# Kernel optimization log

Hardware: AMD Instinct MI355X
Metric: run time of the kernel (lower is better)

Reference implementation:

```python
import jax, jax.numpy as jnp
import numpy as np

B, S, D, H, DFF = 2, 2048, 1024, 16, 4096
DK = D // H
EPS = 1e-5


def layer_norm(x, gamma, beta, eps=EPS):
    mu = jnp.mean(x, axis=-1, keepdims=True)
    var = jnp.mean(jnp.square(x - mu), axis=-1, keepdims=True)
    return (x - mu) * jax.lax.rsqrt(var + eps) * gamma + beta


def setup_inputs() -> dict:
    key = jax.random.key(0)
    ks = jax.random.split(key, 12)
    s_d = 1.0 / np.sqrt(D)
    s_f = 1.0 / np.sqrt(DFF)
    return {
        "x": jax.random.normal(ks[0], (B, S, D), jnp.float32),
        # per-head QKV projections stacked: [H, D, DK]
        "Wq": jax.random.normal(ks[1], (H, D, DK), jnp.float32) * s_d,
        "bq": jnp.zeros((H, DK), jnp.float32),
        "Wk": jax.random.normal(ks[2], (H, D, DK), jnp.float32) * s_d,
        "bk": jnp.zeros((H, DK), jnp.float32),
        "Wv": jax.random.normal(ks[3], (H, D, DK), jnp.float32) * s_d,
        "bv": jnp.zeros((H, DK), jnp.float32),
        "Wo": jax.random.normal(ks[4], (D, D), jnp.float32) * s_d,
        "bo": jnp.zeros((D,), jnp.float32),
        "W1": jax.random.normal(ks[5], (D, DFF), jnp.float32) * s_d,
        "b1": jnp.zeros((DFF,), jnp.float32),
        "W2": jax.random.normal(ks[6], (DFF, D), jnp.float32) * s_f,
        "b2": jnp.zeros((D,), jnp.float32),
        "ln1_g": jnp.ones((D,), jnp.float32),
        "ln1_b": jnp.zeros((D,), jnp.float32),
        "ln2_g": jnp.ones((D,), jnp.float32),
        "ln2_b": jnp.zeros((D,), jnp.float32),
    }


def reference(x, Wq, bq, Wk, bk, Wv, bv, Wo, bo, W1, b1, W2, b2,
              ln1_g, ln1_b, ln2_g, ln2_b):
    # --- residual 1: pre-norm multi-head self-attention (mask unused, dropout=eval) ---
    h = layer_norm(x, ln1_g, ln1_b)                      # [B,S,D]
    q = jnp.einsum('bsd,hdk->bhsk', h, Wq) + bq[:, None, :]
    k = jnp.einsum('bsd,hdk->bhsk', h, Wk) + bk[:, None, :]
    v = jnp.einsum('bsd,hdk->bhsk', h, Wv) + bv[:, None, :]
    scores = jnp.einsum('bhsk,bhtk->bhst', q, k) / np.sqrt(DK)  # [B,H,S,S]
    w = jax.nn.softmax(scores, axis=-1)
    ctx = jnp.einsum('bhst,bhtk->bhsk', w, v)            # [B,H,S,DK]
    # concat heads along feature dim -> [B,S,D]
    ctx = jnp.transpose(ctx, (0, 2, 1, 3)).reshape(B, S, D)
    attn_out = ctx @ Wo + bo
    x = x + attn_out
    # --- residual 2: pre-norm feed-forward ---
    h2 = layer_norm(x, ln2_g, ln2_b)
    ff = jax.nn.relu(h2 @ W1 + b1) @ W2 + b2
    return x + ff
```

## Files before the change

kernel.cpp:

```cpp
#include <hip/hip_runtime.h>

#define B_   2
#define S_   2048
#define D_   1024
#define H_   16
#define DK_  64
#define DFF_ 4096
#define NT_  (B_*S_)
#define QS_  3072

using u16 = unsigned short;
typedef __attribute__((ext_vector_type(8))) short bf16x8;
typedef __attribute__((ext_vector_type(4))) float f32x4;
typedef __attribute__((ext_vector_type(4))) u16  u16x4;

__device__ __forceinline__ float bf2f(u16 h) {
  union { unsigned u; float f; } c; c.u = ((unsigned)h) << 16; return c.f;
}
__device__ __forceinline__ u16 f2bf(float f) {
  union { float f; unsigned u; } c; c.f = f;
  unsigned u = c.u;
  return (u16)((u + 0x7fffu + ((u >> 16) & 1u)) >> 16);
}
__device__ __forceinline__ u16 f2bf_up(float f) {
  union { float f; unsigned u; } c; c.f = f;
  return (u16)((c.u + 0x8000u) >> 16);
}

__device__ __forceinline__ void load_lds16(const void* g, void* l) {
  __builtin_amdgcn_global_load_lds(
      (const __attribute__((address_space(1))) unsigned int*)g,
      (__attribute__((address_space(3))) unsigned int*)l, 16, 0, 0);
}

__device__ __forceinline__ void store_out(u16* p, float v)   { *p = f2bf(v); }
__device__ __forceinline__ void store_out(float* p, float v) { *p = v; }

__global__ __launch_bounds__(256) void ln_kernel(
    const float* __restrict__ x, const float* __restrict__ g,
    const float* __restrict__ bt, u16* __restrict__ o)
{
  const int row = blockIdx.x, t = threadIdx.x;
  const float4 xv = *(const float4*)(x + (size_t)row * D_ + t * 4);
  float f[4] = {xv.x, xv.y, xv.z, xv.w};
  float sum = f[0] + f[1] + f[2] + f[3];
  float sq  = f[0]*f[0] + f[1]*f[1] + f[2]*f[2] + f[3]*f[3];
#pragma unroll
  for (int d = 32; d >= 1; d >>= 1) {
    sum += __shfl_down(sum, d);
    sq  += __shfl_down(sq, d);
  }
  __shared__ float red[8];
  const int lane = t & 63, wid = t >> 6;
  if (lane == 0) { red[wid] = sum; red[wid + 4] = sq; }
  __syncthreads();
  sum = red[0] + red[1] + red[2] + red[3];
  sq  = red[4] + red[5] + red[6] + red[7];
  const float mu   = sum * (1.0f / D_);
  const float var  = sq * (1.0f / D_) - mu * mu;
  const float rstd = rsqrtf(var + 1e-5f);
  const float4 gv = *(const float4*)(g  + t * 4);
  const float4 bv = *(const float4*)(bt + t * 4);
  u16x4 ov;
  ov[0] = f2bf((f[0] - mu) * rstd * gv.x + bv.x);
  ov[1] = f2bf((f[1] - mu) * rstd * gv.y + bv.y);
  ov[2] = f2bf((f[2] - mu) * rstd * gv.z + bv.z);
  ov[3] = f2bf((f[3] - mu) * rstd * gv.w + bv.w);
  *(u16x4*)(o + (size_t)row * D_ + t * 4) = ov;
}

__global__ __launch_bounds__(256) void transpose_h(
    const float* __restrict__ in, u16* __restrict__ out, int R, int C)
{
  __shared__ float tile[32][33];
  const int z = blockIdx.z;
  const float* ip = in  + (size_t)z * R * C;
  u16*         op = out + (size_t)z * R * C;
  const int c0 = blockIdx.x * 32, r0 = blockIdx.y * 32;
  const int tx = threadIdx.x & 31, ty = threadIdx.x >> 5;
#pragma unroll
  for (int i = 0; i < 32; i += 8)
    tile[ty + i][tx] = ip[(size_t)(r0 + ty + i) * C + c0 + tx];
  __syncthreads();
#pragma unroll
  for (int i = 0; i < 32; i += 8)
    op[(size_t)(c0 + ty + i) * R + r0 + tx] = f2bf(tile[tx][ty + i]);
}

__global__ __launch_bounds__(256) void transpose_qkv(
    const float* __restrict__ Wq, const float* __restrict__ Wk,
    const float* __restrict__ Wv, u16* __restrict__ out)
{
  __shared__ float tile[32][33];
  const int z = blockIdx.z;
  const int which = z >> 4, h = z & 15;
  const float* ip = (which == 0 ? Wq : which == 1 ? Wk : Wv) + (size_t)h * 1024 * 64;
  u16* op = out + ((size_t)which * 1024 + h * 64) * 1024;
  const float sc = (which == 0) ? 0.125f : 1.0f;
  const int c0 = blockIdx.x * 32, r0 = blockIdx.y * 32;
  const int tx = threadIdx.x & 31, ty = threadIdx.x >> 5;
#pragma unroll
  for (int i = 0; i < 32; i += 8)
    tile[ty + i][tx] = ip[(size_t)(r0 + ty + i) * 64 + c0 + tx];
  __syncthreads();
#pragma unroll
  for (int i = 0; i < 32; i += 8)
    op[(size_t)(c0 + ty + i) * 1024 + r0 + tx] = f2bf(tile[tx][ty + i] * sc);
}

__global__ __launch_bounds__(256) void transpose_v(
    const u16* __restrict__ qkv, u16* __restrict__ vt)
{
  __shared__ u16 tile[32][33];
  const int z = blockIdx.z;
  const int b = z >> 4, h = z & 15;
  const u16* ip = qkv + (size_t)(b * S_) * QS_ + 2048 + h * DK_;
  u16* op = vt + (size_t)z * DK_ * S_;
  const int t0 = blockIdx.x * 32, d0 = blockIdx.y * 32;
  const int tx = threadIdx.x & 31, ty = threadIdx.x >> 5;
#pragma unroll
  for (int i = 0; i < 32; i += 8)
    tile[ty + i][tx] = ip[(size_t)(t0 + ty + i) * QS_ + d0 + tx];
  __syncthreads();
#pragma unroll
  for (int i = 0; i < 32; i += 8)
    op[(size_t)(d0 + ty + i) * S_ + t0 + tx] = tile[tx][ty + i];
}

template <typename OT, int KK>
__global__ __launch_bounds__(512, 1) void gemm256(
    const u16* __restrict__ A, const u16* __restrict__ Bt,
    const float* __restrict__ bias, const float* __restrict__ biasB,
    const float* __restrict__ biasC, OT* __restrict__ C,
    int M, int N, int do_relu)
{
  constexpr int NK = KK / 32;
  __shared__ u16 lA[4][256 * 32];
  __shared__ u16 lB[4][256 * 32];
  const int tid = threadIdx.x, lane = tid & 63, wid = tid >> 6;
  const int wr = wid >> 2, wc = wid & 3;

  const int nbx = gridDim.x;
  int bid = blockIdx.y * nbx + blockIdx.x;
  const int cpx = (nbx * gridDim.y) >> 3;
  bid = (bid & 7) * cpx + (bid >> 3);
  const int row0 = (bid / nbx) * 256, col0 = (bid % nbx) * 256;

  const int c0 = tid,       sr0 = c0 >> 2, q0 = ((c0 & 3) ^ (((sr0 >> 3) & 1) << 1)) * 8;
  const int c1 = tid + 512, sr1 = c1 >> 2, q1 = ((c1 & 3) ^ (((sr1 >> 3) & 1) << 1)) * 8;
  const u16* As0 = A  + (size_t)(row0 + sr0) * KK + q0;
  const u16* As1 = A  + (size_t)(row0 + sr1) * KK + q1;
  const u16* Bs0 = Bt + (size_t)(col0 + sr0) * KK + q0;
  const u16* Bs1 = Bt + (size_t)(col0 + sr1) * KK + q1;

  f32x4 acc[8][4] = {};
  const int lrow = lane & 15, kcol = (lane >> 4) * 8;

#pragma unroll
  for (int t = 0; t < 3; ++t) {
    load_lds16(As0 + t * 32, &lA[t][c0 * 8]);
    load_lds16(Bs0 + t * 32, &lB[t][c0 * 8]);
    load_lds16(As1 + t * 32, &lA[t][c1 * 8]);
    load_lds16(Bs1 + t * 32, &lB[t][c1 * 8]);
  }
  asm volatile("s_waitcnt vmcnt(8)" ::: "memory");
  __builtin_amdgcn_sched_barrier(0);
  __builtin_amdgcn_s_barrier();

#pragma unroll 4
  for (int j = 0; j < NK; ++j) {
    const int b = j & 3;
    const u16* la = lA[b];
    const u16* lb = lB[b];
    bf16x8 af[4], bfr[4];

#pragma unroll
    for (int m = 0; m < 4; ++m) {
      const int row = wr * 128 + m * 16 + lrow;
      af[m] = *(const bf16x8*)&la[row * 32 + (kcol ^ (((row >> 3) & 1) << 4))];
    }
#pragma unroll
    for (int n = 0; n < 4; ++n) {
      const int row = wc * 64 + n * 16 + lrow;
      bfr[n] = *(const bf16x8*)&lb[row * 32 + (kcol ^ (((row >> 3) & 1) << 4))];
    }
    if (j + 3 < NK) {
      const int bb = (j + 3) & 3;
      load_lds16(As0 + (j + 3) * 32, &lA[bb][c0 * 8]);
      load_lds16(Bs0 + (j + 3) * 32, &lB[bb][c0 * 8]);
    }
    __builtin_amdgcn_s_setprio(1);
#pragma unroll
    for (int m = 0; m < 4; ++m)
#pragma unroll
      for (int n = 0; n < 4; ++n)
        acc[m][n] = __builtin_amdgcn_mfma_f32_16x16x32_bf16(af[m], bfr[n], acc[m][n], 0, 0, 0);
    __builtin_amdgcn_s_setprio(0);
    __builtin_amdgcn_sched_barrier(0);
    __builtin_amdgcn_s_barrier();

#pragma unroll
    for (int m = 0; m < 4; ++m) {
      const int row = wr * 128 + (m + 4) * 16 + lrow;
      af[m] = *(const bf16x8*)&la[row * 32 + (kcol ^ (((row >> 3) & 1) << 4))];
    }
    if (j + 3 < NK) {
      const int bb = (j + 3) & 3;
      load_lds16(As1 + (j + 3) * 32, &lA[bb][c1 * 8]);
      load_lds16(Bs1 + (j + 3) * 32, &lB[bb][c1 * 8]);
    }
    __builtin_amdgcn_s_setprio(1);
#pragma unroll
    for (int m = 0; m < 4; ++m)
#pragma unroll
      for (int n = 0; n < 4; ++n)
        acc[m + 4][n] = __builtin_amdgcn_mfma_f32_16x16x32_bf16(af[m], bfr[n], acc[m + 4][n], 0, 0, 0);
    __builtin_amdgcn_s_setprio(0);
    if (j + 3 < NK)      { asm volatile("s_waitcnt vmcnt(8)" ::: "memory"); }
    else if (j + 2 < NK) { asm volatile("s_waitcnt vmcnt(4)" ::: "memory"); }
    else if (j + 1 < NK) { asm volatile("s_waitcnt vmcnt(0)" ::: "memory"); }
    __builtin_amdgcn_sched_barrier(0);
    __builtin_amdgcn_s_barrier();
  }

#pragma unroll
  for (int m = 0; m < 8; ++m)
#pragma unroll
    for (int n = 0; n < 4; ++n) {
      const int rbase = row0 + wr*128 + m*16 + ((lane >> 4) << 2);
      const int c     = col0 + wc*64 + n*16 + (lane & 15);
      float bv = 0.f;
      if (biasC)      bv = c < 1024 ? bias[c] * 0.125f
                         : (c < 2048 ? biasB[c - 1024] : biasC[c - 2048]);
      else if (bias)  bv = bias[c];
#pragma unroll
      for (int r = 0; r < 4; ++r) {
        float vv = acc[m][n][r] + bv;
        if (do_relu) vv = vv > 0.f ? vv : 0.f;
        store_out(&C[(size_t)(rbase + r) * N + c], vv);
      }
    }
}

template <int KK>
__global__ __launch_bounds__(512, 1) void gemm256pk(
    const u16* __restrict__ A, const u16* __restrict__ Bt,
    u16* __restrict__ P, int M, int N, int Ktot)
{
  constexpr int NK = KK / 32;
  __shared__ u16 lA[4][256 * 32];
  __shared__ u16 lB[4][256 * 32];
  const int tid = threadIdx.x, lane = tid & 63, wid = tid >> 6;
  const int wr = wid >> 2, wc = wid & 3;

  const int nbx = gridDim.x;
  int bid = blockIdx.y * nbx + blockIdx.x;
  const int cpx = (nbx * gridDim.y) >> 3;
  bid = (bid & 7) * cpx + (bid >> 3);
  const int row0 = (bid / nbx) * 256, col0 = (bid % nbx) * 256;
  const int kb = blockIdx.z * KK;

  const int c0 = tid,       sr0 = c0 >> 2, q0 = ((c0 & 3) ^ (((sr0 >> 3) & 1) << 1)) * 8;
  const int c1 = tid + 512, sr1 = c1 >> 2, q1 = ((c1 & 3) ^ (((sr1 >> 3) & 1) << 1)) * 8;
  const u16* As0 = A  + (size_t)(row0 + sr0) * Ktot + kb + q0;
  const u16* As1 = A  + (size_t)(row0 + sr1) * Ktot + kb + q1;
  const u16* Bs0 = Bt + (size_t)(col0 + sr0) * Ktot + kb + q0;
  const u16* Bs1 = Bt + (size_t)(col0 + sr1) * Ktot + kb + q1;

  f32x4 acc[8][4] = {};
  const int lrow = lane & 15, kcol = (lane >> 4) * 8;

#pragma unroll
  for (int t = 0; t < 3; ++t) {
    load_lds16(As0 + t * 32, &lA[t][c0 * 8]);
    load_lds16(Bs0 + t * 32, &lB[t][c0 * 8]);
    load_lds16(As1 + t * 32, &lA[t][c1 * 8]);
    load_lds16(Bs1 + t * 32, &lB[t][c1 * 8]);
  }
  asm volatile("s_waitcnt vmcnt(8)" ::: "memory");
  __builtin_amdgcn_sched_barrier(0);
  __builtin_amdgcn_s_barrier();

#pragma unroll 4
  for (int j = 0; j < NK; ++j) {
    const int b = j & 3;
    const u16* la = lA[b];
    const u16* lb = lB[b];
    bf16x8 af[4], bfr[4];

#pragma unroll
    for (int m = 0; m < 4; ++m) {
      const int row = wr * 128 + m * 16 + lrow;
      af[m] = *(const bf16x8*)&la[row * 32 + (kcol ^ (((row >> 3) & 1) << 4))];
    }
#pragma unroll
    for (int n = 0; n < 4; ++n) {
      const int row = wc * 64 + n * 16 + lrow;
      bfr[n] = *(const bf16x8*)&lb[row * 32 + (kcol ^ (((row >> 3) & 1) << 4))];
    }
    if (j + 3 < NK) {
      const int bb = (j + 3) & 3;
      load_lds16(As0 + (j + 3) * 32, &lA[bb][c0 * 8]);
      load_lds16(Bs0 + (j + 3) * 32, &lB[bb][c0 * 8]);
    }
    __builtin_amdgcn_s_setprio(1);
#pragma unroll
    for (int m = 0; m < 4; ++m)
#pragma unroll
      for (int n = 0; n < 4; ++n)
        acc[m][n] = __builtin_amdgcn_mfma_f32_16x16x32_bf16(af[m], bfr[n], acc[m][n], 0, 0, 0);
    __builtin_amdgcn_s_setprio(0);
    __builtin_amdgcn_sched_barrier(0);
    __builtin_amdgcn_s_barrier();

#pragma unroll
    for (int m = 0; m < 4; ++m) {
      const int row = wr * 128 + (m + 4) * 16 + lrow;
      af[m] = *(const bf16x8*)&la[row * 32 + (kcol ^ (((row >> 3) & 1) << 4))];
    }
    if (j + 3 < NK) {
      const int bb = (j + 3) & 3;
      load_lds16(As1 + (j + 3) * 32, &lA[bb][c1 * 8]);
      load_lds16(Bs1 + (j + 3) * 32, &lB[bb][c1 * 8]);
    }
    __builtin_amdgcn_s_setprio(1);
#pragma unroll
    for (int m = 0; m < 4; ++m)
#pragma unroll
      for (int n = 0; n < 4; ++n)
        acc[m + 4][n] = __builtin_amdgcn_mfma_f32_16x16x32_bf16(af[m], bfr[n], acc[m + 4][n], 0, 0, 0);
    __builtin_amdgcn_s_setprio(0);
    if (j + 3 < NK)      { asm volatile("s_waitcnt vmcnt(8)" ::: "memory"); }
    else if (j + 2 < NK) { asm volatile("s_waitcnt vmcnt(4)" ::: "memory"); }
    else if (j + 1 < NK) { asm volatile("s_waitcnt vmcnt(0)" ::: "memory"); }
    __builtin_amdgcn_sched_barrier(0);
    __builtin_amdgcn_s_barrier();
  }

  u16* Pz = P + (size_t)blockIdx.z * M * N;
#pragma unroll
  for (int m = 0; m < 8; ++m)
#pragma unroll
    for (int n = 0; n < 4; ++n) {
      const int rbase = row0 + wr*128 + m*16 + ((lane >> 4) << 2);
      const int c     = col0 + wc*64 + n*16 + (lane & 15);
#pragma unroll
      for (int r = 0; r < 4; ++r)
        Pz[(size_t)(rbase + r) * N + c] = f2bf(acc[m][n][r]);
    }
}

template <typename OT>
__global__ __launch_bounds__(256) void gemm_bt64(
    const u16* __restrict__ A, const u16* __restrict__ Bt,
    const float* __restrict__ bias, const float* __restrict__ res,
    OT* __restrict__ C, int M, int N, int K, int do_relu)
{
  __shared__ u16 lA[2][128 * 32];
  __shared__ u16 lB[2][64 * 32];
  const int tid = threadIdx.x, lane = tid & 63, wid = tid >> 6;

  const int nbx = gridDim.x;
  int bid = blockIdx.y * nbx + blockIdx.x;
  const int cpx = (nbx * gridDim.y) >> 3;
  bid = (bid & 7) * cpx + (bid >> 3);
  const int row0 = (bid / nbx) * 128, col0 = (bid % nbx) * 64;

  f32x4 acc[2][4] = {};

  const int cc0 = tid, cc1 = tid + 256;
  const int r0 = cc0 >> 2, s0 = cc0 & 3;
  const int r1 = cc1 >> 2, s1 = cc1 & 3;
  const int ko0 = (s0 ^ ((r0 >> 1) & 3)) * 8;
  const int ko1 = (s1 ^ ((r1 >> 1) & 3)) * 8;

#define GST64(bf, k0)                                                         \
  {                                                                           \
    load_lds16(A  + (size_t)(row0 + r0) * K + (k0) + ko0, &lA[bf][cc0 * 8]);  \
    load_lds16(A  + (size_t)(row0 + r1) * K + (k0) + ko1, &lA[bf][cc1 * 8]);  \
    load_lds16(Bt + (size_t)(col0 + r0) * K + (k0) + ko0, &lB[bf][cc0 * 8]);  \
  }

  const int nk = K >> 5;
  GST64(0, 0);
  int cur = 0;
  for (int t = 0; t < nk; ++t) {
    __syncthreads();
    if (t + 1 < nk) GST64(cur ^ 1, (t + 1) * 32);
    bf16x8 af[2], bfr[4];
#pragma unroll
    for (int m = 0; m < 2; ++m) {
      const int row = wid * 32 + m * 16 + (lane & 15);
      af[m] = *(const bf16x8*)&lA[cur][row * 32 + (((lane >> 4) ^ ((row >> 1) & 3)) * 8)];
    }
#pragma unroll
    for (int n = 0; n < 4; ++n) {
      const int row = n * 16 + (lane & 15);
      bfr[n] = *(const bf16x8*)&lB[cur][row * 32 + (((lane >> 4) ^ ((row >> 1) & 3)) * 8)];
    }
#pragma unroll
    for (int m = 0; m < 2; ++m)
#pragma unroll
      for (int n = 0; n < 4; ++n)
        acc[m][n] = __builtin_amdgcn_mfma_f32_16x16x32_bf16(af[m], bfr[n], acc[m][n], 0, 0, 0);
    cur ^= 1;
  }
#undef GST64

#pragma unroll
  for (int m = 0; m < 2; ++m)
#pragma unroll
    for (int n = 0; n < 4; ++n) {
      const int rbase = row0 + wid*32 + m*16 + ((lane >> 4) << 2);
      const int c     = col0 + n*16 + (lane & 15);
      const float bv  = bias ? bias[c] : 0.f;
#pragma unroll
      for (int r = 0; r < 4; ++r) {
        const int rr = rbase + r;
        float vv = acc[m][n][r] + bv;
        if (res) vv += res[(size_t)rr * N + c];
        if (do_relu) vv = vv > 0.f ? vv : 0.f;
        store_out(&C[(size_t)rr * N + c], vv);
      }
    }
}

__global__ __launch_bounds__(256) void ffr_reduce4(
    const u16* __restrict__ P, const float* __restrict__ x1,
    const float* __restrict__ b2, float* __restrict__ out)
{
  const size_t i = (size_t)blockIdx.x * 256 + threadIdx.x;
  const size_t M4 = (size_t)NT_ * D_;
  const float4 r  = ((const float4*)x1)[i];
  const float4 bb = ((const float4*)b2)[i & 255];
  float o0 = r.x + bb.x, o1 = r.y + bb.y, o2 = r.z + bb.z, o3 = r.w + bb.w;
#pragma unroll
  for (int z = 0; z < 4; ++z) {
    const u16x4 p = *(const u16x4*)(P + z * M4 + i * 4);
    o0 += bf2f(p[0]); o1 += bf2f(p[1]); o2 += bf2f(p[2]); o3 += bf2f(p[3]);
  }
  float4 o; o.x = o0; o.y = o1; o.z = o2; o.w = o3;
  ((float4*)out)[i] = o;
}

__global__ __launch_bounds__(512) void attn_kernel(
    const u16* __restrict__ QKV, const u16* __restrict__ Vt, u16* __restrict__ O)
{
  __shared__ u16 lK[2][64 * 64];
  __shared__ u16 lV[2][64 * 64];
  __shared__ u16 lP[128 * 64];

  const int tid = threadIdx.x, lane = tid & 63, wid = tid >> 6;
  const int qt = ((blockIdx.x & 7) << 1) | (blockIdx.x >> 3);
  const int h = blockIdx.y, b = blockIdx.z;

  const u16* Qp = QKV + (size_t)(b * S_ + qt * 128) * QS_ + h * DK_;
  const u16* Kb = QKV + (size_t)(b * S_) * QS_ + 1024 + h * DK_;
  const u16* Vb = Vt  + (size_t)(b * H_ + h) * DK_ * S_;

  bf16x8 qf[2];
  {
    const int qr = wid * 16 + (lane & 15);
    qf[0] = *(const bf16x8*)(Qp + (size_t)qr * QS_ + (lane >> 4) * 8);
    qf[1] = *(const bf16x8*)(Qp + (size_t)qr * QS_ + 32 + (lane >> 4) * 8);
  }

  const bf16x8 vone = {16256,16256,16256,16256,16256,16256,16256,16256};

#define STAGE_KV(bf, kt)                                                      \
  {                                                                           \
    const u16* Kp = Kb + (size_t)(kt) * 64 * QS_;                             \
    const u16* Vp = Vb + (size_t)(kt) * 64;                                   \
    const int c = tid, r = c >> 3, sub = c & 7;                               \
    load_lds16(Kp + (size_t)r * QS_ + ((sub ^ (r & 7)) * 8), &lK[bf][c * 8]); \
    load_lds16(Vp + (size_t)r * S_  + ((sub ^ (r & 7)) * 8), &lV[bf][c * 8]); \
  }

  float m_run = -1e30f;
  f32x4 l_acc = {};
  f32x4 o_acc[4] = {};

  STAGE_KV(0, 0);
  int cur = 0;

  for (int kt = 0; kt < S_ / 64; ++kt) {
    __syncthreads();
    if (kt + 1 < S_ / 64) STAGE_KV(cur ^ 1, kt + 1);

    f32x4 s[4];
    __builtin_amdgcn_s_setprio(1);
#pragma unroll
    for (int kf = 0; kf < 4; ++kf) {
      const int row = kf * 16 + (lane & 15);
      const int i0 = (row * 64 + (lane >> 4) * 8)      ^ ((row & 7) << 3);
      const int i1 = (row * 64 + 32 + (lane >> 4) * 8) ^ ((row & 7) << 3);
      bf16x8 k0 = *(const bf16x8*)&lK[cur][i0];
      bf16x8 k1 = *(const bf16x8*)&lK[cur][i1];
      f32x4 sc = {};
      sc = __builtin_amdgcn_mfma_f32_16x16x32_bf16(k0, qf[0], sc, 0, 0, 0);
      sc = __builtin_amdgcn_mfma_f32_16x16x32_bf16(k1, qf[1], sc, 0, 0, 0);
      s[kf] = sc;
    }
    __builtin_amdgcn_s_setprio(0);

    float t0 = fmaxf(fmaxf(s[0][0], s[0][1]), fmaxf(s[0][2], s[0][3]));
    float t1 = fmaxf(fmaxf(s[1][0], s[1][1]), fmaxf(s[1][2], s[1][3]));
    float t2 = fmaxf(fmaxf(s[2][0], s[2][1]), fmaxf(s[2][2], s[2][3]));
    float t3 = fmaxf(fmaxf(s[3][0], s[3][1]), fmaxf(s[3][2], s[3][3]));
    float pmax = fmaxf(fmaxf(t0, t1), fmaxf(t2, t3));
    pmax = fmaxf(pmax, __shfl_xor(pmax, 16));
    pmax = fmaxf(pmax, __shfl_xor(pmax, 32));

    const bool grow = pmax > m_run + 8.0f;
    const float mnew = grow ? pmax : m_run;
    if (__any(grow)) {
      const float scale = __expf(m_run - mnew);
#pragma unroll
      for (int r = 0; r < 4; ++r) {
        const float sr = __shfl(scale, (lane >> 4) * 4 + r);
        l_acc[r] *= sr;
#pragma unroll
        for (int nf = 0; nf < 4; ++nf) o_acc[nf][r] *= sr;
      }
    }
    m_run = mnew;

    const int prow = wid * 16 + (lane & 15);
#pragma unroll
    for (int kf = 0; kf < 4; ++kf) {
      u16x4 pk;
#pragma unroll
      for (int r = 0; r < 4; ++r) pk[r] = f2bf_up(__expf(s[kf][r] - m_run));
      const int idx = (prow * 64 + kf * 16 + (lane >> 4) * 4) ^ ((prow & 7) << 3);
      *(u16x4*)&lP[idx] = pk;
    }
    asm volatile("s_waitcnt lgkmcnt(0)" ::: "memory");
    __builtin_amdgcn_sched_barrier(0);

    bf16x8 pa0 = *(const bf16x8*)&lP[(prow * 64 + (lane >> 4) * 8)      ^ ((prow & 7) << 3)];
    bf16x8 pa1 = *(const bf16x8*)&lP[(prow * 64 + 32 + (lane >> 4) * 8) ^ ((prow & 7) << 3)];
    __builtin_amdgcn_s_setprio(1);
    l_acc = __builtin_amdgcn_mfma_f32_16x16x32_bf16(pa0, vone, l_acc, 0, 0, 0);
    l_acc = __builtin_amdgcn_mfma_f32_16x16x32_bf16(pa1, vone, l_acc, 0, 0, 0);
#pragma unroll
    for (int nf = 0; nf < 4; ++nf) {
      const int vrow = nf * 16 + (lane & 15);
      bf16x8 v0 = *(const bf16x8*)&lV[cur][(vrow * 64 + (lane >> 4) * 8)      ^ ((vrow & 7) << 3)];
      bf16x8 v1 = *(const bf16x8*)&lV[cur][(vrow * 64 + 32 + (lane >> 4) * 8) ^ ((vrow & 7) << 3)];
      o_acc[nf] = __builtin_amdgcn_mfma_f32_16x16x32_bf16(pa0, v0, o_acc[nf], 0, 0, 0);
      o_acc[nf] = __builtin_amdgcn_mfma_f32_16x16x32_bf16(pa1, v1, o_acc[nf], 0, 0, 0);
    }
    __builtin_amdgcn_s_setprio(0);
    cur ^= 1;
  }

#pragma unroll
  for (int nf = 0; nf < 4; ++nf)
#pragma unroll
    for (int r = 0; r < 4; ++r) {
      const int qrow = qt * 128 + wid * 16 + (lane >> 4) * 4 + r;
      const int col  = h * DK_ + nf * 16 + (lane & 15);
      O[(size_t)(b * S_ + qrow) * D_ + col] = f2bf(o_acc[nf][r] / l_acc[r]);
    }
}

extern "C" void kernel_launch(void* const* d_in, const int* in_sizes, int n_in,
                              void* d_out, int out_size, void* d_ws, size_t ws_size,
                              hipStream_t stream)
{
  const float* x   = (const float*)d_in[0];
  const float* Wq  = (const float*)d_in[1];
  const float* bq  = (const float*)d_in[2];
  const float* Wk  = (const float*)d_in[3];
  const float* bk  = (const float*)d_in[4];
  const float* Wv  = (const float*)d_in[5];
  const float* bv  = (const float*)d_in[6];
  const float* Wo  = (const float*)d_in[7];
  const float* bo  = (const float*)d_in[8];
  const float* W1  = (const float*)d_in[9];
  const float* b1  = (const float*)d_in[10];
  const float* W2  = (const float*)d_in[11];
  const float* b2  = (const float*)d_in[12];
  const float* g1  = (const float*)d_in[13];
  const float* be1 = (const float*)d_in[14];
  const float* g2  = (const float*)d_in[15];
  const float* be2 = (const float*)d_in[16];
  float* out = (float*)d_out;

  const size_t MB = 1024 * 1024;
  char* base = (char*)d_ws;
  u16*   xn    = (u16*)(base);
  u16*   qkv   = (u16*)(base +  8*MB);
  u16*   ctx   = (u16*)(base + 32*MB);
  float* x1    = (float*)(base + 40*MB);
  u16*   vt    = (u16*)(base + 40*MB);
  u16*   ff1   = (u16*)(base +  8*MB);
  u16*   wqkvT = (u16*)(base + 56*MB);
  u16*   woT   = (u16*)(base + 62*MB);
  u16*   w1T   = (u16*)(base + 64*MB);
  u16*   w2T   = (u16*)(base + 72*MB);
  u16*   pkh   = (u16*)(base + 80*MB);

  const bool splitk = ws_size >= (size_t)112 * MB;

  dim3 blk(256);
  transpose_qkv<<<dim3(2, 32, 48), blk, 0, stream>>>(Wq, Wk, Wv, wqkvT);
  transpose_h<<<dim3(32, 32, 1),  blk, 0, stream>>>(Wo, woT, 1024, 1024);
  transpose_h<<<dim3(128, 32, 1), blk, 0, stream>>>(W1, w1T, 1024, 4096);
  transpose_h<<<dim3(32, 128, 1), blk, 0, stream>>>(W2, w2T, 4096, 1024);

  ln_kernel<<<NT_, blk, 0, stream>>>(x, g1, be1, xn);

  gemm256<u16, 1024><<<dim3(12, 16), dim3(512), 0, stream>>>(
      xn, wqkvT, bq, bk, bv, qkv, NT_, QS_, 0);

  transpose_v<<<dim3(64, 2, 32), blk, 0, stream>>>(qkv, vt);

  attn_kernel<<<dim3(S_ / 128, H_, B_), dim3(512), 0, stream>>>(qkv, vt, ctx);

  gemm_bt64<<<dim3(16, 32), blk, 0, stream>>>(ctx, woT, bo, x, x1, NT_, D_, D_, 0);

  ln_kernel<<<NT_, blk, 0, stream>>>(x1, g2, be2, xn);

  gemm256<u16, 1024><<<dim3(16, 16), dim3(512), 0, stream>>>(
      xn, w1T, b1, (const float*)nullptr, (const float*)nullptr, ff1, NT_, DFF_, 1);

  if (splitk) {
    gemm256pk<1024><<<dim3(4, 16, 4), dim3(512), 0, stream>>>(
        ff1, w2T, pkh, NT_, D_, DFF_);
    ffr_reduce4<<<dim3(4096), blk, 0, stream>>>(pkh, x1, b2, out);
  } else {
    gemm_bt64<<<dim3(16, 32), blk, 0, stream>>>(ff1, w2T, b2, x1, out, NT_, D_, DFF_, 0);
  }
}
```

Before: 260.1 us.

## Pack K into contiguous per-head buffer and remap attention grid

Replaces the V-only transpose kernel with pack_kv, which also copies K into a contiguous per-(batch,head) [S,64] buffer and transposes V using 16-byte vector loads and stores. The attention kernel now streams K tiles from that compact buffer instead of strided QKV rows. Its grid becomes 1D with a remapped block index that spreads heads and batches across the launch, aiming at better cache and L2 locality. This costs an extra 8MB of K writes in the workspace at 48MB, which must not collide with the other buffers.

```diff
diff --git a/kernel.cpp b/kernel.cpp
--- a/kernel.cpp
+++ b/kernel.cpp
@@ -108,23 +108,27 @@
     op[(size_t)(c0 + ty + i) * 1024 + r0 + tx] = f2bf(tile[tx][ty + i] * sc);
 }
 
-__global__ __launch_bounds__(256) void transpose_v(
-    const u16* __restrict__ qkv, u16* __restrict__ vt)
-{
-  __shared__ u16 tile[32][33];
-  const int z = blockIdx.z;
+__global__ __launch_bounds__(256) void pack_kv(
+    const u16* __restrict__ qkv, u16* __restrict__ kt, u16* __restrict__ vt)
+{
+  __shared__ u16 tile[32][72];
+  const int z = blockIdx.y;
   const int b = z >> 4, h = z & 15;
-  const u16* ip = qkv + (size_t)(b * S_) * QS_ + 2048 + h * DK_;
-  u16* op = vt + (size_t)z * DK_ * S_;
-  const int t0 = blockIdx.x * 32, d0 = blockIdx.y * 32;
-  const int tx = threadIdx.x & 31, ty = threadIdx.x >> 5;
-#pragma unroll
-  for (int i = 0; i < 32; i += 8)
-    tile[ty + i][tx] = ip[(size_t)(t0 + ty + i) * QS_ + d0 + tx];
+  const int t0 = blockIdx.x * 32;
+  const int tid = threadIdx.x;
+  const int row = tid >> 3, sub = tid & 7;
+
+  const u16* src = qkv + (size_t)(b * S_ + t0 + row) * QS_ + h * DK_ + sub * 8;
+  *(bf16x8*)(kt + ((size_t)z * S_ + t0 + row) * 64 + sub * 8) =
+      *(const bf16x8*)(src + 1024);
+  *(bf16x8*)&tile[row][sub * 8] = *(const bf16x8*)(src + 2048);
   __syncthreads();
-#pragma unroll
-  for (int i = 0; i < 32; i += 8)
-    op[(size_t)(d0 + ty + i) * S_ + t0 + tx] = tile[tx][ty + i];
+
+  const int d = tid >> 2, tc = (tid & 3) * 8;
+  bf16x8 val;
+#pragma unroll
+  for (int j = 0; j < 8; ++j) val[j] = (short)tile[tc + j][d];
+  *(bf16x8*)(vt + ((size_t)z * 64 + d) * S_ + t0 + tc) = val;
 }
 
 template <typename OT, int KK>
@@ -444,19 +448,21 @@
 }
 
 __global__ __launch_bounds__(512) void attn_kernel(
-    const u16* __restrict__ QKV, const u16* __restrict__ Vt, u16* __restrict__ O)
+    const u16* __restrict__ QKV, const u16* __restrict__ Kt,
+    const u16* __restrict__ Vt, u16* __restrict__ O)
 {
   __shared__ u16 lK[2][64 * 64];
   __shared__ u16 lV[2][64 * 64];
   __shared__ u16 lP[128 * 64];
 
   const int tid = threadIdx.x, lane = tid & 63, wid = tid >> 6;
-  const int qt = ((blockIdx.x & 7) << 1) | (blockIdx.x >> 3);
-  const int h = blockIdx.y, b = blockIdx.z;
-
-  const u16* Qp = QKV + (size_t)(b * S_ + qt * 128) * QS_ + h * DK_;
-  const u16* Kb = QKV + (size_t)(b * S_) * QS_ + 1024 + h * DK_;
-  const u16* Vb = Vt  + (size_t)(b * H_ + h) * DK_ * S_;
+  const int g  = (blockIdx.x & 7) * 64 + (blockIdx.x >> 3);
+  const int qt = g & 15, h = (g >> 4) & 15, b = g >> 8;
+  const int z  = b * H_ + h;
+
+  const u16* Qp  = QKV + (size_t)(b * S_ + qt * 128) * QS_ + h * DK_;
+  const u16* Kpb = Kt + (size_t)z * S_ * 64;
+  const u16* Vb  = Vt + (size_t)z * DK_ * S_;
 
   bf16x8 qf[2];
   {
@@ -467,13 +473,13 @@
 
   const bf16x8 vone = {16256,16256,16256,16256,16256,16256,16256,16256};
 
-#define STAGE_KV(bf, kt)                                                      \
+#define STAGE_KV(bf, kt_)                                                     \
   {                                                                           \
-    const u16* Kp = Kb + (size_t)(kt) * 64 * QS_;                             \
-    const u16* Vp = Vb + (size_t)(kt) * 64;                                   \
+    const u16* Kp = Kpb + (size_t)(kt_) * 64 * 64;                            \
+    const u16* Vp = Vb + (size_t)(kt_) * 64;                                  \
     const int c = tid, r = c >> 3, sub = c & 7;                               \
-    load_lds16(Kp + (size_t)r * QS_ + ((sub ^ (r & 7)) * 8), &lK[bf][c * 8]); \
-    load_lds16(Vp + (size_t)r * S_  + ((sub ^ (r & 7)) * 8), &lV[bf][c * 8]); \
+    load_lds16(Kp + r * 64 + ((sub ^ (r & 7)) * 8), &lK[bf][c * 8]);          \
+    load_lds16(Vp + (size_t)r * S_ + ((sub ^ (r & 7)) * 8), &lV[bf][c * 8]);  \
   }
 
   float m_run = -1e30f;
@@ -594,6 +600,7 @@
   u16*   ctx   = (u16*)(base + 32*MB);
   float* x1    = (float*)(base + 40*MB);
   u16*   vt    = (u16*)(base + 40*MB);
+  u16*   kt    = (u16*)(base + 48*MB);
   u16*   ff1   = (u16*)(base +  8*MB);
   u16*   wqkvT = (u16*)(base + 56*MB);
   u16*   woT   = (u16*)(base + 62*MB);
@@ -614,9 +621,9 @@
   gemm256<u16, 1024><<<dim3(12, 16), dim3(512), 0, stream>>>(
       xn, wqkvT, bq, bk, bv, qkv, NT_, QS_, 0);
 
-  transpose_v<<<dim3(64, 2, 32), blk, 0, stream>>>(qkv, vt);
-
-  attn_kernel<<<dim3(S_ / 128, H_, B_), dim3(512), 0, stream>>>(qkv, vt, ctx);
+  pack_kv<<<dim3(S_ / 32, B_ * H_), blk, 0, stream>>>(qkv, kt, vt);
+
+  attn_kernel<<<dim3(512), dim3(512), 0, stream>>>(qkv, kt, vt, ctx);
 
   gemm_bt64<<<dim3(16, 32), blk, 0, stream>>>(ctx, woT, bo, x, x1, NT_, D_, D_, 0);
 
```

Result: no change. 260.3 us (+0.1%).
